# Optimization experiments

Hardware: AMD Instinct MI355X
Metric: run time of the kernel (lower is better)

## Reference

```python
import jax, jax.numpy as jnp
import numpy as np

GRID = 30
S = GRID * GRID            # 900 cells
D = 512                    # embed_dim
HQ = 8                     # query heads
HKV = 2                    # kv heads (GQA)
DH = D // HQ               # 64 head dim
T = 16                     # history length


def _rope_pairwise_1d(x, pos, inv_freq):
    """RoPE on adjacent pairs. x: (L,H,d), pos: (L,), inv_freq: (d//2,)."""
    theta = pos[:, None] * inv_freq[None, :]          # (L, d//2)
    cos = jnp.cos(theta)[:, None, :]                  # (L,1,d//2)
    sin = jnp.sin(theta)[:, None, :]
    xr, xi = x[..., 0::2], x[..., 1::2]               # even/odd pairs (= view(L,H,-1,2))
    out = jnp.stack((xr * cos - xi * sin, xr * sin + xi * cos), axis=-1)
    return out.reshape(x.shape)


def _rope_2d(x, coords_xy, inv_x, inv_y):
    """2D RoPE: first half rotated by x-coord, second half by y-coord."""
    d_axis = x.shape[-1] // 2
    x_part = _rope_pairwise_1d(x[..., :d_axis], coords_xy[:, 0], inv_x)
    y_part = _rope_pairwise_1d(x[..., d_axis:], coords_xy[:, 1], inv_y)
    return jnp.concatenate((x_part, y_part), axis=-1)


def setup_inputs() -> dict:
    key = jax.random.key(0)
    ks = jax.random.split(key, 7)
    sc = 1.0 / np.sqrt(D)
    return {
        "static_grid": jax.random.normal(ks[0], (GRID, GRID, D), jnp.float32),
        "history_seq": jax.random.normal(ks[1], (T, GRID, GRID, D), jnp.float32),
        "init_embed": jax.random.normal(ks[2], (D,), jnp.float32),
        "Wq": jax.random.normal(ks[3], (D, D), jnp.float32) * sc,
        "Wk": jax.random.normal(ks[4], (HKV * DH, D), jnp.float32) * sc,
        "Wv": jax.random.normal(ks[5], (HKV * DH, D), jnp.float32) * sc,
        "Wo": jax.random.normal(ks[6], (D, D), jnp.float32) * sc,
    }


def reference(static_grid, history_seq, init_embed, Wq, Wk, Wv, Wo):
    dtype = static_grid.dtype
    quarter, half = DH // 4, DH // 2
    inv_2d = 1.0 / (10000.0 ** (jnp.arange(quarter, dtype=dtype) / quarter))  # (dh//4,)
    inv_1d = 1.0 / (10000.0 ** (jnp.arange(half, dtype=dtype) / half))        # (dh//2,)

    gy, gx = jnp.meshgrid(jnp.arange(GRID), jnp.arange(GRID), indexing="ij")
    coords = jnp.stack((gy, gx), axis=-1).reshape(S, 2).astype(dtype)          # (S,2)

    cur = static_grid.reshape(S, D)                    # current frame tokens
    hist = history_seq.reshape(T * S, D)               # per-cell histories
    # token order: [learnable_init, cell_histories (t=0..T-1), current_grid]
    tokens = jnp.concatenate((init_embed[None, :], hist, cur), axis=0)  # (Lkv, D)

    tok_pos = jnp.concatenate((
        jnp.zeros((1,), dtype),
        jnp.repeat(jnp.arange(T, dtype=dtype), S),
        jnp.full((S,), T, dtype=dtype),
    ))                                                  # (Lkv,) temporal positions
    tok_coords = jnp.concatenate((
        jnp.zeros((1, 2), dtype),
        jnp.tile(coords, (T, 1)),
        coords,
    ), axis=0)                                          # (Lkv,2)

    # projections (queries only for the current frame; output is the updated frame)
    q = (cur @ Wq.T).reshape(S, HQ, DH)
    k = (tokens @ Wk.T).reshape(-1, HKV, DH)
    v = (tokens @ Wv.T).reshape(-1, HKV, DH)

    # fused temporal(1D) + spatial(2D) RoPE on q and k
    q = _rope_2d(_rope_pairwise_1d(q, jnp.full((S,), T, dtype=dtype), inv_1d), coords, inv_2d, inv_2d)
    k = _rope_2d(_rope_pairwise_1d(k, tok_pos, inv_1d), tok_coords, inv_2d, inv_2d)

    # grouped-query attention: expand kv heads
    g = HQ // HKV
    k = jnp.repeat(k, g, axis=1)                        # (Lkv, HQ, DH)
    v = jnp.repeat(v, g, axis=1)

    scores = jnp.einsum("qhd,khd->hqk", q, k) / jnp.sqrt(jnp.asarray(DH, dtype))

    # pedestal mask: attend to init + own temporal column + all current cells
    cell = jnp.arange(S)
    hist_cell = jnp.tile(cell, T)                       # (T*S,)
    mask = jnp.concatenate((
        jnp.ones((S, 1), bool),
        cell[:, None] == hist_cell[None, :],
        jnp.ones((S, S), bool),
    ), axis=1)                                          # (S, Lkv)
    scores = jnp.where(mask[None], scores, jnp.finfo(dtype).min)

    attn = jax.nn.softmax(scores, axis=-1)
    out = jnp.einsum("hqk,khd->qhd", attn, v).reshape(S, D)
    return (out @ Wo.T).reshape(GRID, GRID, D)
```

## Files before the change

### kernel.cpp

```cpp
#include <hip/hip_runtime.h>
#include <math.h>

static constexpr int GRIDN = 30;
static constexpr int S    = 900;
static constexpr int D    = 512;
static constexpr int HQ   = 8;
static constexpr int HKV  = 2;
static constexpr int T    = 16;
static constexpr int NTOK = 1 + T*S + S;
static constexpr int CUR0 = 1 + T*S;

static constexpr int THROWS = 15360;
static constexpr int VTC    = 960;
static constexpr int PBS    = 952;
static constexpr int LSTR   = 72;

typedef _Float16 half8  __attribute__((ext_vector_type(8)));
typedef _Float16 half4  __attribute__((ext_vector_type(4)));
typedef __fp16   fp16x2 __attribute__((ext_vector_type(2)));
typedef float    floatx4 __attribute__((ext_vector_type(4)));

#define MFMA16(a,b,c) __builtin_amdgcn_mfma_f32_16x16x32_f16((a),(b),(c),0,0,0)

#if defined(__has_builtin)
#if __has_builtin(__builtin_amdgcn_fdot2)
#define HAVE_FDOT2 1
#endif
#endif

__device__ __forceinline__ half8 to_half8(float4 a, float4 b) {
    half8 h;
    h[0]=(_Float16)a.x; h[1]=(_Float16)a.y; h[2]=(_Float16)a.z; h[3]=(_Float16)a.w;
    h[4]=(_Float16)b.x; h[5]=(_Float16)b.y; h[6]=(_Float16)b.z; h[7]=(_Float16)b.w;
    return h;
}

__device__ __forceinline__ half4 cvt4(float4 a) {
    const fp16x2 p0 = __builtin_amdgcn_cvt_pkrtz(a.x, a.y);
    const fp16x2 p1 = __builtin_amdgcn_cvt_pkrtz(a.z, a.w);
    half4 h;
    h[0]=(_Float16)p0[0]; h[1]=(_Float16)p0[1];
    h[2]=(_Float16)p1[0]; h[3]=(_Float16)p1[1];
    return h;
}

__global__ __launch_bounds__(256) void prep_w(
    const float* __restrict__ Wq, const float* __restrict__ Wk,
    const float* __restrict__ Wv, const float* __restrict__ Wo,
    _Float16* __restrict__ Wqh, _Float16* __restrict__ Whkv,
    _Float16* __restrict__ Woh)
{
    const size_t i8 = ((size_t)blockIdx.x * 256 + threadIdx.x) * 8;
    const float* src; _Float16* dst; size_t off;
    if (i8 < 262144)      { src = Wq; dst = Wqh;          off = i8; }
    else if (i8 < 327680) { src = Wk; dst = Whkv;         off = i8 - 262144; }
    else if (i8 < 393216) { src = Wv; dst = Whkv + 65536; off = i8 - 327680; }
    else                  { src = Wo; dst = Woh;          off = i8 - 393216; }
    const float4 f0 = *(const float4*)(src + off);
    const float4 f1 = *(const float4*)(src + off + 4);
    *(half8*)(dst + off) = to_half8(f0, f1);
}

__global__ __launch_bounds__(256) void proj(
    const float* __restrict__ init_e, const float* __restrict__ hist,
    const float* __restrict__ cur,
    const _Float16* __restrict__ Whkv, const _Float16* __restrict__ Wqh,
    _Float16* __restrict__ Kh, _Float16* __restrict__ Vh,
    _Float16* __restrict__ Vt, _Float16* __restrict__ Qh)
{
    __shared__ _Float16 Alds[2][32 * LSTR];
    __shared__ _Float16 Blds[2][128 * LSTR];

    const int tid  = threadIdx.x;
    const int w    = tid >> 6, lane = tid & 63;
    const int r    = lane & 15, kb = lane >> 4;
    const int ww   = w >> 1, wc = w & 1;
    const int bx   = blockIdx.x;
    const bool isQ = (bx >= 960);

    int l0, n0, bc;
    const _Float16* Wb;
    if (!isQ) { l0 = (bx >> 1) * 32;               bc = bx & 1;  n0 = bc * 128; Wb = Whkv; }
    else      { const int qb = bx - 960;
                l0 = CUR0 + (qb >> 2) * 32;        bc = qb & 3;  n0 = bc * 128; Wb = Wqh; }

    const float* arow[2];
    #pragma unroll
    for (int j = 0; j < 2; ++j) {
        int l = l0 + j * 16 + (tid >> 4);
        if (l >= NTOK) l = 0;
        const float* rp = (l == 0) ? init_e
                        : (l <= T*S ? hist + (size_t)(l - 1) * 512
                                    : cur  + (size_t)(l - CUR0) * 512);
        arow[j] = rp + (tid & 15) * 4;
    }
    const _Float16* brow[4];
    #pragma unroll
    for (int j = 0; j < 4; ++j)
        brow[j] = Wb + (size_t)(n0 + j * 32 + (tid >> 3)) * 512 + (tid & 7) * 8;

    float4 areg[2];
    half8  breg[4];

    floatx4 acc[4] = {};

    #pragma unroll
    for (int j = 0; j < 2; ++j) areg[j] = *(const float4*)arow[j];
    #pragma unroll
    for (int j = 0; j < 4; ++j) breg[j] = *(const half8*)brow[j];
    #pragma unroll
    for (int j = 0; j < 2; ++j)
        *(half4*)&Alds[0][(j*16 + (tid >> 4)) * LSTR + (tid & 15) * 4] = cvt4(areg[j]);
    #pragma unroll
    for (int j = 0; j < 4; ++j)
        *(half8*)&Blds[0][(j*32 + (tid >> 3)) * LSTR + (tid & 7) * 8]  = breg[j];
    __syncthreads();

    for (int c = 0; c < 8; ++c) {
        const int buf = c & 1;
        if (c < 7) {
            const int k0 = (c + 1) * 64;
            #pragma unroll
            for (int j = 0; j < 2; ++j) areg[j] = *(const float4*)(arow[j] + k0);
            #pragma unroll
            for (int j = 0; j < 4; ++j) breg[j] = *(const half8*)(brow[j] + k0);
        }
        #pragma unroll
        for (int s = 0; s < 2; ++s) {
            const half8 a = *(const half8*)&Alds[buf][(ww*16 + r) * LSTR + s*32 + kb*8];
            #pragma unroll
            for (int nt = 0; nt < 4; ++nt) {
                const half8 b = *(const half8*)&Blds[buf][(wc*64 + nt*16 + r) * LSTR + s*32 + kb*8];
                acc[nt] = MFMA16(a, b, acc[nt]);
            }
        }
        if (c < 7) {
            __syncthreads();
            #pragma unroll
            for (int j = 0; j < 2; ++j)
                *(half4*)&Alds[buf ^ 1][(j*16 + (tid >> 4)) * LSTR + (tid & 15) * 4] = cvt4(areg[j]);
            #pragma unroll
            for (int j = 0; j < 4; ++j)
                *(half8*)&Blds[buf ^ 1][(j*32 + (tid >> 3)) * LSTR + (tid & 7) * 8]  = breg[j];
            __syncthreads();
        }
    }

    const float LN1E4 = 9.210340371976184f;
    float inv1[4], inv2[4]; int jj[4];
    #pragma unroll
    for (int nt = 0; nt < 4; ++nt) {
        const int cl = nt * 16 + r;
        jj[nt] = cl >> 1;
        inv1[nt] = __expf(-(float)jj[nt]        * (LN1E4 / 32.f));
        inv2[nt] = __expf(-(float)(jj[nt] & 15) * (LN1E4 / 16.f));
    }

    if (!isQ) {
        if (bc == 0) {
            #pragma unroll
            for (int i = 0; i < 4; ++i) {
                const int l = l0 + ww*16 + kb*4 + i;
                float pos, cy, cx;
                if (l == 0) { pos = 0.f; cy = 0.f; cx = 0.f; }
                else if (l <= T*S) {
                    const int j2 = l - 1;
                    const int t_ = j2 / S;
                    const int cell = j2 - t_ * S;
                    pos = (float)t_;
                    cy = (float)(cell / GRIDN); cx = (float)(cell % GRIDN);
                } else {
                    const int cell = l - CUR0;
                    pos = (float)T;
                    cy = (float)(cell / GRIDN); cx = (float)(cell % GRIDN);
                }
                #pragma unroll
                for (int nt = 0; nt < 4; ++nt) {
                    const float own = acc[nt][i];
                    const float oth = __shfl_xor(own, 1);
                    const float c2 = (jj[nt] < 16) ? cy : cx;
                    const float theta = pos * inv1[nt] + c2 * inv2[nt];
                    float sn, cs; __sincosf(theta, &sn, &cs);
                    const int cc = wc*64 + nt*16 + r;
                    const float o = ((cc & 1) == 0) ? (own * cs - oth * sn)
                                                    : (oth * sn + own * cs);
                    if (l < NTOK) Kh[(size_t)l * 128 + cc] = (_Float16)o;
                }
            }
        } else {
            #pragma unroll
            for (int nt = 0; nt < 4; ++nt) {
                const int vd = wc*64 + nt*16 + r;
                #pragma unroll
                for (int i = 0; i < 4; ++i) {
                    const int l = l0 + ww*16 + kb*4 + i;
                    if (l >= NTOK) continue;
                    const _Float16 hv = (_Float16)acc[nt][i];
                    Vh[(size_t)l * 128 + vd] = hv;
                    const int cc = l - CUR0;
                    if (cc >= 0 && cc < S)
                        Vt[(size_t)vd * VTC + cc] = hv;
                }
            }
        }
    } else {
        #pragma unroll
        for (int i = 0; i < 4; ++i) {
            const int l = l0 + ww*16 + kb*4 + i;
            const int s = l - CUR0;
            const int ssafe = (s < S) ? s : 0;
            const float cy = (float)(ssafe / GRIDN), cx = (float)(ssafe % GRIDN);
            #pragma unroll
            for (int nt = 0; nt < 4; ++nt) {
                const float own = acc[nt][i];
                const float oth = __shfl_xor(own, 1);
                const float c2 = (jj[nt] < 16) ? cy : cx;
                const float theta = 16.f * inv1[nt] + c2 * inv2[nt];
                float sn, cs; __sincosf(theta, &sn, &cs);
                const int C = bc*128 + wc*64 + nt*16 + r;
                const float o = ((C & 1) == 0) ? (own * cs - oth * sn)
                                               : (oth * sn + own * cs);
                if (s < S)
                    Qh[(size_t)s * 512 + C] = (_Float16)(o * 0.125f);
            }
        }
    }
}

__global__ __launch_bounds__(512) void attn_f16(
    const _Float16* __restrict__ Qh, const _Float16* __restrict__ Kh,
    const _Float16* __restrict__ Vt, const _Float16* __restrict__ Vh,
    _Float16* __restrict__ Oh)
{
    __shared__ _Float16 pb[16][PBS];
    __shared__ float ex[16][20];
    __shared__ float wpm[8][16], wps[8][16];
    __shared__ float rowm[16], rowinv[16];
    __shared__ float Oe[16][68];
    __shared__ float Op[2][16][68];

    const int q0  = blockIdx.x * 16;
    const int h   = blockIdx.y;
    const int kvh = h >> 2;
    const int tid = threadIdx.x;
    const int w = tid >> 6, lane = tid & 63;
    const int r = lane & 15, g = lane >> 4;

    {
        const int er = tid & 15;
        const int e  = tid >> 4;
        if (e < 17) {
            const int s  = q0 + er;
            const int ss = (s < S) ? s : 0;
            const _Float16* qp = Qh + (size_t)(q0 + er) * 512 + h * 64;
            const int l = (e == 0) ? 0 : (1 + (e - 1) * S + ss);
            const _Float16* kp = Kh + (size_t)l * 128 + kvh * 64;
            float acc = 0.f;
            #pragma unroll
            for (int d8 = 0; d8 < 8; ++d8) {
                const half8 qv = *(const half8*)(qp + d8 * 8);
                const half8 kv = *(const half8*)(kp + d8 * 8);
#ifdef HAVE_FDOT2
                #pragma unroll
                for (int p_ = 0; p_ < 4; ++p_) {
                    fp16x2 qq; qq[0] = (__fp16)qv[2*p_]; qq[1] = (__fp16)qv[2*p_+1];
                    fp16x2 kk; kk[0] = (__fp16)kv[2*p_]; kk[1] = (__fp16)kv[2*p_+1];
                    acc = __builtin_amdgcn_fdot2(qq, kk, acc, false);
                }
#else
                #pragma unroll
                for (int q_ = 0; q_ < 8; ++q_)
                    acc += (float)qv[q_] * (float)kv[q_];
#endif
            }
            ex[er][e] = acc;
        }
    }

    half8 qa[2];
    #pragma unroll
    for (int ks = 0; ks < 2; ++ks)
        qa[ks] = *(const half8*)(Qh + (size_t)(q0 + r) * 512 + h * 64 + ks * 32 + g * 8);

    floatx4 qacc[8];
    #pragma unroll
    for (int t = 0; t < 8; ++t) {
        const int nt = w + 8 * t;
        floatx4 a = {0.f, 0.f, 0.f, 0.f};
        if (nt <= 56) {
            const _Float16* kp = Kh + (size_t)(CUR0 + nt * 16 + r) * 128 + kvh * 64 + g * 8;
            a = MFMA16(qa[0], *(const half8*)kp, a);
            a = MFMA16(qa[1], *(const half8*)(kp + 32), a);
        }
        qacc[t] = a;
    }

    float pm[4] = {-1e30f, -1e30f, -1e30f, -1e30f};
    #pragma unroll
    for (int t = 0; t < 8; ++t) {
        const int nt = w + 8 * t;
        const bool valid = (nt <= 56) && !((nt == 56) && (r >= 4));
        #pragma unroll
        for (int i = 0; i < 4; ++i)
            if (valid) pm[i] = fmaxf(pm[i], qacc[t][i]);
    }
    #pragma unroll
    for (int m = 1; m < 16; m <<= 1)
        #pragma unroll
        for (int i = 0; i < 4; ++i)
            pm[i] = fmaxf(pm[i], __shfl_xor(pm[i], m));
    if (r == 0)
        #pragma unroll
        for (int i = 0; i < 4; ++i) wpm[w][g * 4 + i] = pm[i];
    __syncthreads();

    if (tid < 16) {
        float m = wpm[0][tid];
        #pragma unroll
        for (int w2 = 1; w2 < 8; ++w2) m = fmaxf(m, wpm[w2][tid]);
        #pragma unroll
        for (int e = 0; e < 17; ++e) m = fmaxf(m, ex[tid][e]);
        rowm[tid] = m;
    }
    __syncthreads();

    {
        const int er = tid & 15;
        const int e  = tid >> 4;
        if (e < 17) ex[er][e] = __expf(ex[er][e] - rowm[er]);
    }
    if (tid < 256) pb[tid >> 4][912 + (tid & 15)] = (_Float16)0.f;

    float ps[4] = {0.f, 0.f, 0.f, 0.f};
    #pragma unroll
    for (int t = 0; t < 8; ++t) {
        const int nt = w + 8 * t;
        if (nt <= 56) {
            const int c = nt * 16 + r;
            const bool masked = (nt == 56) && (r >= 4);
            #pragma unroll
            for (int i = 0; i < 4; ++i) {
                const int row = g * 4 + i;
                const float e = masked ? 0.f : __expf(qacc[t][i] - rowm[row]);
                ps[i] += e;
                pb[row][c] = (_Float16)e;
            }
        }
    }
    #pragma unroll
    for (int m = 1; m < 16; m <<= 1)
        #pragma unroll
        for (int i = 0; i < 4; ++i) ps[i] += __shfl_xor(ps[i], m);
    if (r == 0)
        #pragma unroll
        for (int i = 0; i < 4; ++i) wps[w][g * 4 + i] = ps[i];
    __syncthreads();

    if (tid < 16) {
        float s_ = wps[0][tid];
        #pragma unroll
        for (int w2 = 1; w2 < 8; ++w2) s_ += wps[w2][tid];
        #pragma unroll
        for (int e = 0; e < 17; ++e) s_ += ex[tid][e];
        rowinv[tid] = 1.f / s_;
    }
    __syncthreads();

    if (tid < 256) {
        const int er = tid & 15, gg = tid >> 4;
        const int s  = q0 + er;
        const int ss = (s < S) ? s : 0;
        float o0 = 0.f, o1 = 0.f, o2 = 0.f, o3 = 0.f;
        for (int e = 0; e < 17; ++e) {
            const int l = (e == 0) ? 0 : (1 + (e - 1) * S + ss);
            const float p = ex[er][e];
            const half4 v = *(const half4*)(Vh + (size_t)l * 128 + kvh * 64 + gg * 4);
            o0 = fmaf(p, (float)v[0], o0); o1 = fmaf(p, (float)v[1], o1);
            o2 = fmaf(p, (float)v[2], o2); o3 = fmaf(p, (float)v[3], o3);
        }
        *(float4*)&Oe[er][gg * 4] = make_float4(o0, o1, o2, o3);
    }

    const int d0 = (w & 3) * 16;
    const int kh = w >> 2;
    floatx4 oa = {0.f, 0.f, 0.f, 0.f};
    const _Float16* vrow = Vt + ((size_t)kvh * 64 + d0 + r) * VTC + g * 8;
    const int ks0 = kh ? 15 : 0;
    const int ks1 = kh ? 29 : 15;
    for (int ks = ks0; ks < ks1; ++ks) {
        const half8 pf = *(const half8*)(&pb[r][ks * 32 + g * 8]);
        const half8 vf = *(const half8*)(vrow + ks * 32);
        oa = MFMA16(pf, vf, oa);
    }
    #pragma unroll
    for (int i = 0; i < 4; ++i)
        Op[kh][g * 4 + i][d0 + r] = oa[i];
    __syncthreads();

    if (tid < 256) {
        #pragma unroll
        for (int i = 0; i < 4; ++i) {
            const int row = g * 4 + i;
            const int s = q0 + row;
            if (s < S) {
                const float o = (Op[0][row][w * 16 + r] + Op[1][row][w * 16 + r]
                               + Oe[row][w * 16 + r]) * rowinv[row];
                Oh[(size_t)s * 512 + h * 64 + w * 16 + r] = (_Float16)o;
            }
        }
    }
}

__global__ __launch_bounds__(256) void gemm_out(
    const _Float16* __restrict__ A, const _Float16* __restrict__ Wh,
    float* __restrict__ Out, int M)
{
    const int tid = threadIdx.x;
    const int w = tid >> 6, lane = tid & 63;
    const int r = lane & 15, kb = lane >> 4;
    const int l0 = blockIdx.x * 32;
    const int n0 = blockIdx.y * 256 + w*64;

    const _Float16* ap[2];
    #pragma unroll
    for (int mt = 0; mt < 2; ++mt)
        ap[mt] = A + (size_t)(l0 + mt*16 + r)*512 + kb*8;
    const _Float16* bp[4];
    #pragma unroll
    for (int nt = 0; nt < 4; ++nt)
        bp[nt] = Wh + (size_t)(n0 + nt*16 + r) * 512 + kb*8;

    floatx4 acc[2][4] = {};
    #pragma unroll 2
    for (int k0 = 0; k0 < 512; k0 += 32) {
        half8 a[2], b[4];
        #pragma unroll
        for (int mt = 0; mt < 2; ++mt) a[mt] = *(const half8*)(ap[mt] + k0);
        #pragma unroll
        for (int nt = 0; nt < 4; ++nt) b[nt] = *(const half8*)(bp[nt] + k0);
        #pragma unroll
        for (int mt = 0; mt < 2; ++mt)
            #pragma unroll
            for (int nt = 0; nt < 4; ++nt)
                acc[mt][nt] = MFMA16(a[mt], b[nt], acc[mt][nt]);
    }
    #pragma unroll
    for (int mt = 0; mt < 2; ++mt)
        #pragma unroll
        for (int nt = 0; nt < 4; ++nt)
            #pragma unroll
            for (int i = 0; i < 4; ++i) {
                const int l = l0 + mt*16 + kb*4 + i;
                if (l < M)
                    Out[(size_t)l*512 + n0 + nt*16 + r] = acc[mt][nt][i];
            }
}

extern "C" void kernel_launch(void* const* d_in, const int* in_sizes, int n_in,
                              void* d_out, int out_size, void* d_ws, size_t ws_size,
                              hipStream_t stream)
{
    (void)in_sizes; (void)n_in; (void)out_size; (void)ws_size;
    const float* static_grid = (const float*)d_in[0];
    const float* history     = (const float*)d_in[1];
    const float* init_embed  = (const float*)d_in[2];
    const float* Wq = (const float*)d_in[3];
    const float* Wk = (const float*)d_in[4];
    const float* Wv = (const float*)d_in[5];
    const float* Wo = (const float*)d_in[6];
    float* out = (float*)d_out;

    char* p = (char*)d_ws;
    _Float16* Wqh  = (_Float16*)p;  p += (size_t)262144 * 2;
    _Float16* Whkv = (_Float16*)p;  p += (size_t)131072 * 2;
    _Float16* Woh  = (_Float16*)p;  p += (size_t)262144 * 2;
    _Float16* Kh   = (_Float16*)p;  p += (size_t)THROWS * 128 * 2;
    _Float16* Vh   = (_Float16*)p;  p += (size_t)THROWS * 128 * 2;
    _Float16* Vt   = (_Float16*)p;  p += (size_t)2 * 64 * VTC * 2;
    _Float16* Qh   = (_Float16*)p;  p += (size_t)928 * 512 * 2;
    _Float16* Oh   = (_Float16*)p;  p += (size_t)928 * 512 * 2;

    prep_w<<<320, 256, 0, stream>>>(Wq, Wk, Wv, Wo, Wqh, Whkv, Woh);
    proj<<<1076, 256, 0, stream>>>(init_embed, history, static_grid,
                                   Whkv, Wqh, Kh, Vh, Vt, Qh);
    attn_f16<<<dim3(57, 8), 512, 0, stream>>>(Qh, Kh, Vt, Vh, Oh);
    gemm_out<<<dim3(29, 2), 256, 0, stream>>>(Oh, Woh, out, S);
}
```

Before: 136.6 us.

## Widen proj tiles to 256 columns with 512 threads, single-buffer LDS

The projection kernel now gives each block 32 rows by 256 output columns with 8 waves, so the K and V halves (or a Q half) come from one block instead of two. Each activation row is loaded and converted once instead of twice, which cuts redundant reads of the large history tensor. LDS double buffering is dropped in favour of a single buffer. That keeps shared memory in check but serialises the LDS store with the compute, which could expose more latency.

```diff
diff --git a/kernel.cpp b/kernel.cpp
--- a/kernel.cpp
+++ b/kernel.cpp
@@ -61,87 +61,80 @@
     *(half8*)(dst + off) = to_half8(f0, f1);
 }
 
-__global__ __launch_bounds__(256) void proj(
+__global__ __launch_bounds__(512) void proj(
     const float* __restrict__ init_e, const float* __restrict__ hist,
     const float* __restrict__ cur,
     const _Float16* __restrict__ Whkv, const _Float16* __restrict__ Wqh,
     _Float16* __restrict__ Kh, _Float16* __restrict__ Vh,
     _Float16* __restrict__ Vt, _Float16* __restrict__ Qh)
 {
-    __shared__ _Float16 Alds[2][32 * LSTR];
-    __shared__ _Float16 Blds[2][128 * LSTR];
+    __shared__ _Float16 Alds[32 * LSTR];
+    __shared__ _Float16 Blds[256 * LSTR];
 
     const int tid  = threadIdx.x;
     const int w    = tid >> 6, lane = tid & 63;
     const int r    = lane & 15, kb = lane >> 4;
-    const int ww   = w >> 1, wc = w & 1;
+    const int ww   = w >> 2, wc = w & 3;
     const int bx   = blockIdx.x;
-    const bool isQ = (bx >= 960);
-
-    int l0, n0, bc;
+    const bool isQ = (bx >= 479);
+
+    int l0, n0;
     const _Float16* Wb;
-    if (!isQ) { l0 = (bx >> 1) * 32;               bc = bx & 1;  n0 = bc * 128; Wb = Whkv; }
-    else      { const int qb = bx - 960;
-                l0 = CUR0 + (qb >> 2) * 32;        bc = qb & 3;  n0 = bc * 128; Wb = Wqh; }
-
-    const float* arow[2];
-    #pragma unroll
-    for (int j = 0; j < 2; ++j) {
-        int l = l0 + j * 16 + (tid >> 4);
+    int bc = 0;
+    if (!isQ) { l0 = bx * 32;                    n0 = 0;        Wb = Whkv; }
+    else      { const int qb = bx - 479;
+                l0 = CUR0 + (qb >> 1) * 32;      bc = qb & 1;   n0 = bc * 256; Wb = Wqh; }
+
+    const float* arow;
+    {
+        int l = l0 + (tid >> 4);
         if (l >= NTOK) l = 0;
         const float* rp = (l == 0) ? init_e
                         : (l <= T*S ? hist + (size_t)(l - 1) * 512
                                     : cur  + (size_t)(l - CUR0) * 512);
-        arow[j] = rp + (tid & 15) * 4;
+        arow = rp + (tid & 15) * 4;
     }
     const _Float16* brow[4];
     #pragma unroll
     for (int j = 0; j < 4; ++j)
-        brow[j] = Wb + (size_t)(n0 + j * 32 + (tid >> 3)) * 512 + (tid & 7) * 8;
-
-    float4 areg[2];
+        brow[j] = Wb + (size_t)(n0 + j * 64 + (tid >> 3)) * 512 + (tid & 7) * 8;
+
+    float4 areg;
     half8  breg[4];
 
     floatx4 acc[4] = {};
 
-    #pragma unroll
-    for (int j = 0; j < 2; ++j) areg[j] = *(const float4*)arow[j];
+    areg = *(const float4*)arow;
     #pragma unroll
     for (int j = 0; j < 4; ++j) breg[j] = *(const half8*)brow[j];
-    #pragma unroll
-    for (int j = 0; j < 2; ++j)
-        *(half4*)&Alds[0][(j*16 + (tid >> 4)) * LSTR + (tid & 15) * 4] = cvt4(areg[j]);
+    *(half4*)&Alds[(tid >> 4) * LSTR + (tid & 15) * 4] = cvt4(areg);
     #pragma unroll
     for (int j = 0; j < 4; ++j)
-        *(half8*)&Blds[0][(j*32 + (tid >> 3)) * LSTR + (tid & 7) * 8]  = breg[j];
+        *(half8*)&Blds[(j * 64 + (tid >> 3)) * LSTR + (tid & 7) * 8] = breg[j];
     __syncthreads();
 
     for (int c = 0; c < 8; ++c) {
-        const int buf = c & 1;
         if (c < 7) {
             const int k0 = (c + 1) * 64;
-            #pragma unroll
-            for (int j = 0; j < 2; ++j) areg[j] = *(const float4*)(arow[j] + k0);
+            areg = *(const float4*)(arow + k0);
             #pragma unroll
             for (int j = 0; j < 4; ++j) breg[j] = *(const half8*)(brow[j] + k0);
         }
         #pragma unroll
         for (int s = 0; s < 2; ++s) {
-            const half8 a = *(const half8*)&Alds[buf][(ww*16 + r) * LSTR + s*32 + kb*8];
+            const half8 a = *(const half8*)&Alds[(ww*16 + r) * LSTR + s*32 + kb*8];
             #pragma unroll
             for (int nt = 0; nt < 4; ++nt) {
-                const half8 b = *(const half8*)&Blds[buf][(wc*64 + nt*16 + r) * LSTR + s*32 + kb*8];
+                const half8 b = *(const half8*)&Blds[(wc*64 + nt*16 + r) * LSTR + s*32 + kb*8];
                 acc[nt] = MFMA16(a, b, acc[nt]);
             }
         }
         if (c < 7) {
             __syncthreads();
-            #pragma unroll
-            for (int j = 0; j < 2; ++j)
-                *(half4*)&Alds[buf ^ 1][(j*16 + (tid >> 4)) * LSTR + (tid & 15) * 4] = cvt4(areg[j]);
+            *(half4*)&Alds[(tid >> 4) * LSTR + (tid & 15) * 4] = cvt4(areg);
             #pragma unroll
             for (int j = 0; j < 4; ++j)
-                *(half8*)&Blds[buf ^ 1][(j*32 + (tid >> 3)) * LSTR + (tid & 7) * 8]  = breg[j];
+                *(half8*)&Blds[(j * 64 + (tid >> 3)) * LSTR + (tid & 7) * 8] = breg[j];
             __syncthreads();
         }
     }
@@ -157,7 +150,7 @@
     }
 
     if (!isQ) {
-        if (bc == 0) {
+        if (wc < 2) {
             #pragma unroll
             for (int i = 0; i < 4; ++i) {
                 const int l = l0 + ww*16 + kb*4 + i;
@@ -190,7 +183,7 @@
         } else {
             #pragma unroll
             for (int nt = 0; nt < 4; ++nt) {
-                const int vd = wc*64 + nt*16 + r;
+                const int vd = (wc - 2)*64 + nt*16 + r;
                 #pragma unroll
                 for (int i = 0; i < 4; ++i) {
                     const int l = l0 + ww*16 + kb*4 + i;
@@ -217,7 +210,7 @@
                 const float c2 = (jj[nt] < 16) ? cy : cx;
                 const float theta = 16.f * inv1[nt] + c2 * inv2[nt];
                 float sn, cs; __sincosf(theta, &sn, &cs);
-                const int C = bc*128 + wc*64 + nt*16 + r;
+                const int C = bc*256 + wc*64 + nt*16 + r;
                 const float o = ((C & 1) == 0) ? (own * cs - oth * sn)
                                                : (oth * sn + own * cs);
                 if (s < S)
@@ -481,8 +474,8 @@
     _Float16* Oh   = (_Float16*)p;  p += (size_t)928 * 512 * 2;
 
     prep_w<<<320, 256, 0, stream>>>(Wq, Wk, Wv, Wo, Wqh, Whkv, Woh);
-    proj<<<1076, 256, 0, stream>>>(init_embed, history, static_grid,
-                                   Whkv, Wqh, Kh, Vh, Vt, Qh);
+    proj<<<537, 512, 0, stream>>>(init_embed, history, static_grid,
+                                  Whkv, Wqh, Kh, Vh, Vt, Qh);
     attn_f16<<<dim3(57, 8), 512, 0, stream>>>(Qh, Kh, Vt, Vh, Oh);
     gemm_out<<<dim3(29, 2), 256, 0, stream>>>(Oh, Woh, out, S);
 }
```

Result: slower. 140.0 us (+2.5%).
